# Optimization experiments

Hardware: AMD Instinct MI355X
Metric: run time of the kernel (lower is better)

The kernel has to match this reference:

```python
import jax, jax.numpy as jnp
import numpy as np

B, S, D = 4, 2048, 512
H, DK, DV = 8, 64, 64
DFF = 2048
LN_EPS = 1e-5


def _layernorm(x, g, b):
    mu = jnp.mean(x, axis=-1, keepdims=True)
    var = jnp.mean(jnp.square(x - mu), axis=-1, keepdims=True)
    return (x - mu) * jax.lax.rsqrt(var + LN_EPS) * g + b


def setup_inputs() -> dict:
    key = jax.random.key(0)
    ks = jax.random.split(key, 9)
    def xavier(k, shape):
        fan_out, fan_in = shape
        std = np.sqrt(2.0 / (fan_in + fan_out))
        return jax.random.normal(k, shape, jnp.float32) * std
    GELU_GAIN = 1.85
    return {
        "x": jax.random.normal(ks[0], (B, S, D), jnp.float32),
        "attention_mask": jax.random.randint(ks[1], (B, S), 0, 2).astype(bool),
        "Wq": xavier(ks[2], (H * DK, D)),
        "Wk": xavier(ks[3], (H * DK, D)),
        "Wv": xavier(ks[4], (H * DV, D)),
        "Wp": xavier(ks[5], (D, H * DV)),
        "W1": xavier(ks[6], (DFF, D)) * GELU_GAIN,
        "b1": jnp.zeros((DFF,), jnp.float32),
        "W2": xavier(ks[7], (D, DFF)),
        "b2": jnp.zeros((D,), jnp.float32),
        "ln1_g": jnp.ones((D,), jnp.float32),
        "ln1_b": jnp.zeros((D,), jnp.float32),
        "ln2_g": jnp.ones((D,), jnp.float32),
        "ln2_b": jnp.zeros((D,), jnp.float32),
    }


def reference(x, attention_mask, Wq, Wk, Wv, Wp, W1, b1, W2, b2,
              ln1_g, ln1_b, ln2_g, ln2_b):
    b, s, d = x.shape
    residual = x
    q = (x @ Wq.T).reshape(b, s, H, DK)  # [B,S,H,DK]
    k = (x @ Wk.T).reshape(b, s, H, DK)
    v = (x @ Wv.T).reshape(b, s, H, DV)
    score = jnp.einsum("bshd,bthd->bhst", q, k) * (DK ** -0.5)  # [B,H,S,S]
    # subtractive mask: score -= 100 * not(mask)
    score = score - 100.0 * (~attention_mask)[:, None, None, :].astype(score.dtype)
    p = jax.nn.softmax(score, axis=-1)
    ctx = jnp.einsum("bhst,bthd->bshd", p, v).reshape(b, s, H * DV)
    att = ctx @ Wp.T  # dropout p=0.1 is identity in eval
    h = _layernorm(att + residual, ln1_g, ln1_b)
    ff = jax.nn.gelu(h @ W1.T + b1, approximate=False) @ W2.T + b2
    out = _layernorm(ff + h, ln2_g, ln2_b)
    return out
```

## Files before the change

kernel.cpp:

```cpp
#include <hip/hip_runtime.h>
#include <cstdint>
#include <cstddef>

#define B_ 4
#define S_ 2048
#define D_ 512
#define H_ 8
#define DK_ 64
#define DFF_ 2048

using s16x8  = __attribute__((ext_vector_type(8))) short;
using bf16x8 = __attribute__((ext_vector_type(8))) __bf16;
using f32x4  = __attribute__((ext_vector_type(4))) float;

__device__ __forceinline__ short f2bf(float f) {
  unsigned u = __builtin_bit_cast(unsigned, f);
  u += 0x7FFFu + ((u >> 16) & 1u);
  return (short)(u >> 16);
}
__device__ __forceinline__ float bf2f(short s) {
  unsigned u = ((unsigned)(unsigned short)s) << 16;
  return __builtin_bit_cast(float, u);
}

__device__ __forceinline__ void gl2lds16(const void* g, void* l) {
  __builtin_amdgcn_global_load_lds(
      (const __attribute__((address_space(1))) void*)g,
      (__attribute__((address_space(3))) void*)l, 16, 0, 0);
}

__global__ __launch_bounds__(256)
void cvt_all(const float* __restrict__ x, const float* __restrict__ Wq,
             const float* __restrict__ Wk, const float* __restrict__ Wv,
             const float* __restrict__ Wp, const float* __restrict__ W1,
             const float* __restrict__ W2,
             short* __restrict__ xb, short* __restrict__ wqkv,
             short* __restrict__ wp, short* __restrict__ w1, short* __restrict__ w2) {
  int blk = blockIdx.x;
  const float* src; short* dst; int off;
  if (blk < 4096)      { src = x;  dst = xb;            off = blk; }
  else if (blk < 4352) { src = Wq; dst = wqkv;          off = blk - 4096; }
  else if (blk < 4608) { src = Wk; dst = wqkv + 262144; off = blk - 4352; }
  else if (blk < 4864) { src = Wv; dst = wqkv + 524288; off = blk - 4608; }
  else if (blk < 5120) { src = Wp; dst = wp;            off = blk - 4864; }
  else if (blk < 6144) { src = W1; dst = w1;            off = blk - 5120; }
  else                 { src = W2; dst = w2;            off = blk - 6144; }
  int i = (off * 256 + threadIdx.x) * 4;
  float4 v = *(const float4*)(src + i);
  *(short4*)(dst + i) = make_short4(f2bf(v.x), f2bf(v.y), f2bf(v.z), f2bf(v.w));
}

template <int MODE>
__global__ __launch_bounds__(256)
void gemm_bt(const short* __restrict__ A, const short* __restrict__ B,
             int M, int N, int K,
             const float* __restrict__ aux1,
             void* __restrict__ out0, void* __restrict__ out1, void* __restrict__ out2) {
  __shared__ alignas(16) short As[2][128][64];
  __shared__ alignas(16) short Bs[2][128][64];

  const int tid  = threadIdx.x;
  const int lane = tid & 63;
  const int wave = tid >> 6;
  const int quad = lane >> 4;
  const int l16  = lane & 15;
  const int wm   = (wave >> 1) * 64;
  const int wn   = (wave & 1) * 64;
  const int bm   = blockIdx.x * 128;
  const int bn   = blockIdx.y * 128;
  const int Kh   = K / gridDim.z;
  const int koff = blockIdx.z * Kh;

  const int srow8 = lane >> 3;
  const int pb    = lane & 7;

  f32x4 acc[4][4] = {};

  const int nt = Kh >> 6;

#pragma unroll
  for (int i = 0; i < 4; ++i) {
    const int rr = wave * 32 + i * 8 + srow8;
    const int cb = pb ^ (rr & 7);
    gl2lds16(A + (size_t)(bm + rr) * K + koff + cb * 8, &As[0][wave * 32 + i * 8][0]);
    gl2lds16(B + (size_t)(bn + rr) * K + koff + cb * 8, &Bs[0][wave * 32 + i * 8][0]);
  }
  __syncthreads();

  int cur = 0;
  for (int t = 0; t < nt; ++t) {
    if (t + 1 < nt) {
      const int kk = koff + (t + 1) * 64;
#pragma unroll
      for (int i = 0; i < 4; ++i) {
        const int rr = wave * 32 + i * 8 + srow8;
        const int cb = pb ^ (rr & 7);
        gl2lds16(A + (size_t)(bm + rr) * K + kk + cb * 8, &As[cur ^ 1][wave * 32 + i * 8][0]);
        gl2lds16(B + (size_t)(bn + rr) * K + kk + cb * 8, &Bs[cur ^ 1][wave * 32 + i * 8][0]);
      }
    }

#pragma unroll
    for (int c = 0; c < 2; ++c) {
      bf16x8 a[4], b[4];
#pragma unroll
      for (int i = 0; i < 4; ++i) {
        const int row = wm + i * 16 + l16;
        const int pba = (c * 4 + quad) ^ (row & 7);
        a[i] = __builtin_bit_cast(bf16x8, *(const s16x8*)&As[cur][row][pba * 8]);
      }
#pragma unroll
      for (int j = 0; j < 4; ++j) {
        const int row = wn + j * 16 + l16;
        const int pbb = (c * 4 + quad) ^ (row & 7);
        b[j] = __builtin_bit_cast(bf16x8, *(const s16x8*)&Bs[cur][row][pbb * 8]);
      }
#pragma unroll
      for (int i = 0; i < 4; ++i)
#pragma unroll
        for (int j = 0; j < 4; ++j)
          acc[i][j] = __builtin_amdgcn_mfma_f32_16x16x32_bf16(a[i], b[j], acc[i][j], 0, 0, 0);
    }

    __syncthreads();
    cur ^= 1;
  }

#pragma unroll
  for (int i = 0; i < 4; ++i) {
    const int m0 = bm + wm + i * 16 + quad * 4;
#pragma unroll
    for (int j = 0; j < 4; ++j) {
      const int n = bn + wn + j * 16 + l16;
      if constexpr (MODE == 0) {
        const int bb = m0 >> 11, ss0 = m0 & 2047;
        if (n < 512) {
          short4 pk = make_short4(f2bf(acc[i][j][0] * 0.18033688f), f2bf(acc[i][j][1] * 0.18033688f),
                                  f2bf(acc[i][j][2] * 0.18033688f), f2bf(acc[i][j][3] * 0.18033688f));
          *(short4*)((short*)out0 +
              ((((size_t)bb * H_ + (n >> 6)) * 64 + (n & 63)) * S_ + ss0)) = pk;
        } else if (n >= 1024) {
          const int nn = n - 1024;
          short4 pk = make_short4(f2bf(acc[i][j][0]), f2bf(acc[i][j][1]),
                                  f2bf(acc[i][j][2]), f2bf(acc[i][j][3]));
          *(short4*)((short*)out2 +
              ((((size_t)bb * H_ + (nn >> 6)) * 64 + (nn & 63)) * S_ + ss0)) = pk;
        } else {
          const int nn = n - 512;
          const size_t rowb = ((size_t)bb * H_ + (nn >> 6)) * S_ + ss0;
#pragma unroll
          for (int rr = 0; rr < 4; ++rr)
            ((short*)out1)[(rowb + rr) * 64 + (nn & 63)] = f2bf(acc[i][j][rr]);
        }
      } else if constexpr (MODE == 1) {
        float* dst = (float*)out0 + (size_t)blockIdx.z * M * N;
#pragma unroll
        for (int rr = 0; rr < 4; ++rr)
          dst[(size_t)(m0 + rr) * N + n] = acc[i][j][rr];
      } else {
#pragma unroll
        for (int rr = 0; rr < 4; ++rr) {
          float t = acc[i][j][rr] + aux1[n];
          float x2 = t * t;
          float t2 = t * (2.3022082f + 0.1029464f * x2);
          float e  = __builtin_amdgcn_exp2f(t2);
          float gl = t - t * __builtin_amdgcn_rcpf(1.0f + e);
          ((short*)out0)[(size_t)(m0 + rr) * N + n] = f2bf(gl);
        }
      }
    }
  }
}

__global__ __launch_bounds__(512)
void flash_attn_mfma(const short* __restrict__ QTg, const short* __restrict__ Kb,
                     const short* __restrict__ Vtg, const void* __restrict__ mraw,
                     short* __restrict__ ctxb) {
  __shared__ alignas(16) short Ks[64][64];
  __shared__ alignas(16) short Vt[64][64];
  __shared__ alignas(16) short Ps[8][32][64];
  __shared__ alignas(8) unsigned char mbits8[256];
  __shared__ unsigned red[8];

  int flat = (blockIdx.z * 8 + blockIdx.y) * 8 + blockIdx.x;
  flat = (flat & 7) * 32 + (flat >> 3);
  const int b = flat >> 6, h = (flat >> 3) & 7;
  const int q0 = (flat & 7) * 256;

  const int tid = threadIdx.x;
  const int w = tid >> 6, lane = tid & 63;
  const int quad = lane >> 4, l16 = lane & 15;
  const size_t base  = ((size_t)(b * H_ + h)) * S_ * DK_;
  const size_t baseT = ((size_t)(b * H_ + h)) * DK_ * S_;

  {
    const unsigned* mw = (const unsigned*)mraw;
    unsigned v = 0;
#pragma unroll
    for (int i = 0; i < 4; ++i) v |= mw[tid + i * 512];
#pragma unroll
    for (int s = 1; s < 64; s <<= 1) v |= __shfl_xor(v, s);
    if (lane == 0) red[w] = v;
    __syncthreads();
    unsigned f = red[0] | red[1] | red[2] | red[3] |
                 red[4] | red[5] | red[6] | red[7];
    if (tid < 256) {
      unsigned byte = 0;
#pragma unroll
      for (int j = 0; j < 8; ++j) {
        int t = tid * 8 + j;
        int gidx = b * S_ + t;
        int val;
        if ((f & ~1u) == 0u)            val = ((const int*)mraw)[gidx];
        else if (f == 0x3F800000u)      val = (((const float*)mraw)[gidx] != 0.0f);
        else                            val = ((const unsigned char*)mraw)[gidx];
        byte |= (val ? 1u : 0u) << j;
      }
      mbits8[tid] = (unsigned char)byte;
    }
  }

  bf16x8 qa[2][2];
#pragma unroll
  for (int st = 0; st < 2; ++st) {
    const int q = q0 + w * 32 + st * 16 + l16;
#pragma unroll
    for (int c = 0; c < 2; ++c) {
      s16x8 t;
#pragma unroll
      for (int j = 0; j < 8; ++j)
        t[j] = QTg[baseT + (size_t)(c * 32 + quad * 8 + j) * S_ + q];
      qa[st][c] = __builtin_bit_cast(bf16x8, t);
    }
  }

  f32x4 Oc[2][4] = {};
  float li[2] = {};
  const int swz = l16 & 7;

  const int r = tid >> 3, cc = tid & 7;
  const short* kp = Kb  + base  + (size_t)r * 64 + cc * 8;
  const short* vp = Vtg + baseT + (size_t)r * S_ + cc * 8;
  const int ch = ((cc ^ (r & 7)) << 3);

  s16x8 kr = *(const s16x8*)(kp);
  s16x8 vr = *(const s16x8*)(vp);

  for (int t0 = 0; t0 < S_; t0 += 64) {
    __syncthreads();
    *(s16x8*)&Ks[r][ch] = kr;
    *(s16x8*)&Vt[r][ch] = vr;
    __syncthreads();

    if (t0 + 64 < S_) {
      kr = *(const s16x8*)(kp + (size_t)(t0 + 64) * 64);
      vr = *(const s16x8*)(vp + (t0 + 64));
    }

    f32x4 sc[2][4] = {};
    __builtin_amdgcn_s_setprio(1);
#pragma unroll
    for (int c = 0; c < 2; ++c) {
#pragma unroll
      for (int jt = 0; jt < 4; ++jt) {
        bf16x8 kb = __builtin_bit_cast(bf16x8,
            *(const s16x8*)&Ks[jt * 16 + l16][((c * 4 + quad) ^ swz) << 3]);
        sc[0][jt] = __builtin_amdgcn_mfma_f32_16x16x32_bf16(kb, qa[0][c], sc[0][jt], 0, 0, 0);
        sc[1][jt] = __builtin_amdgcn_mfma_f32_16x16x32_bf16(kb, qa[1][c], sc[1][jt], 0, 0, 0);
      }
    }
    __builtin_amdgcn_s_setprio(0);

    const unsigned long long mball =
        *(const unsigned long long*)&mbits8[t0 >> 3];
#pragma unroll
    for (int jt = 0; jt < 4; ++jt) {
      const unsigned m16 = ((unsigned)(mball >> (jt * 16))) >> (quad * 4);
      const int pch = (((jt * 2 + (quad >> 1)) ^ swz) << 3) + (quad & 1) * 4;
#pragma unroll
      for (int st = 0; st < 2; ++st) {
        unsigned uu[4];
#pragma unroll
        for (int rr = 0; rr < 4; ++rr) {
          float pe = __builtin_amdgcn_exp2f(sc[st][jt][rr]);
          unsigned u = __builtin_bit_cast(unsigned, pe) & 0xFFFF0000u;
          u = ((m16 >> rr) & 1u) ? u : 0u;
          li[st] += __builtin_bit_cast(float, u);
          uu[rr] = u;
        }
        *(uint2*)&Ps[w][st * 16 + l16][pch] =
            make_uint2(__builtin_amdgcn_perm(uu[1], uu[0], 0x07060302u),
                       __builtin_amdgcn_perm(uu[3], uu[2], 0x07060302u));
      }
    }

    __builtin_amdgcn_s_setprio(1);
#pragma unroll
    for (int c = 0; c < 2; ++c) {
      bf16x8 pa0 = __builtin_bit_cast(bf16x8,
          *(const s16x8*)&Ps[w][l16][((c * 4 + quad) ^ swz) << 3]);
      bf16x8 pa1 = __builtin_bit_cast(bf16x8,
          *(const s16x8*)&Ps[w][16 + l16][((c * 4 + quad) ^ swz) << 3]);
#pragma unroll
      for (int dt = 0; dt < 4; ++dt) {
        bf16x8 vb = __builtin_bit_cast(bf16x8,
            *(const s16x8*)&Vt[dt * 16 + l16][((c * 4 + quad) ^ swz) << 3]);
        Oc[0][dt] = __builtin_amdgcn_mfma_f32_16x16x32_bf16(pa0, vb, Oc[0][dt], 0, 0, 0);
        Oc[1][dt] = __builtin_amdgcn_mfma_f32_16x16x32_bf16(pa1, vb, Oc[1][dt], 0, 0, 0);
      }
    }
    __builtin_amdgcn_s_setprio(0);
  }

#pragma unroll
  for (int st = 0; st < 2; ++st) {
    float l = li[st];
    l += __shfl_xor(l, 16);
    l += __shfl_xor(l, 32);
#pragma unroll
    for (int rr = 0; rr < 4; ++rr) {
      float lr = __shfl(l, quad * 4 + rr);
      float inv = 1.f / lr;
      const size_t row = (size_t)b * S_ + q0 + w * 32 + st * 16 + quad * 4 + rr;
#pragma unroll
      for (int dt = 0; dt < 4; ++dt)
        ctxb[row * (H_ * DK_) + h * 64 + dt * 16 + l16] = f2bf(Oc[st][dt][rr] * inv);
    }
  }
}

__global__ __launch_bounds__(256)
void ln_fused(const float* __restrict__ p0, const float* __restrict__ p1,
              const float* __restrict__ xres, const short* __restrict__ hres,
              const float* __restrict__ bias,
              const float* __restrict__ g, const float* __restrict__ bb,
              float* __restrict__ out32, short* __restrict__ outb) {
  const int wave = threadIdx.x >> 6, lane = threadIdx.x & 63;
  const int token = blockIdx.x * 4 + wave;
  const size_t off = (size_t)token * D_;
  const int c = lane * 8;

  float v[8];
  {
    float4 a0 = *(const float4*)(p0 + off + c);
    float4 a1 = *(const float4*)(p0 + off + c + 4);
    float4 b0 = *(const float4*)(p1 + off + c);
    float4 b1 = *(const float4*)(p1 + off + c + 4);
    v[0]=a0.x+b0.x; v[1]=a0.y+b0.y; v[2]=a0.z+b0.z; v[3]=a0.w+b0.w;
    v[4]=a1.x+b1.x; v[5]=a1.y+b1.y; v[6]=a1.z+b1.z; v[7]=a1.w+b1.w;
  }
  if (xres) {
    float4 x0 = *(const float4*)(xres + off + c);
    float4 x1 = *(const float4*)(xres + off + c + 4);
    v[0]+=x0.x; v[1]+=x0.y; v[2]+=x0.z; v[3]+=x0.w;
    v[4]+=x1.x; v[5]+=x1.y; v[6]+=x1.z; v[7]+=x1.w;
  }
  if (hres) {
    short4 h0 = *(const short4*)(hres + off + c);
    short4 h1 = *(const short4*)(hres + off + c + 4);
    v[0]+=bf2f(h0.x); v[1]+=bf2f(h0.y); v[2]+=bf2f(h0.z); v[3]+=bf2f(h0.w);
    v[4]+=bf2f(h1.x); v[5]+=bf2f(h1.y); v[6]+=bf2f(h1.z); v[7]+=bf2f(h1.w);
  }
  if (bias) {
    float4 c0 = *(const float4*)(bias + c);
    float4 c1 = *(const float4*)(bias + c + 4);
    v[0]+=c0.x; v[1]+=c0.y; v[2]+=c0.z; v[3]+=c0.w;
    v[4]+=c1.x; v[5]+=c1.y; v[6]+=c1.z; v[7]+=c1.w;
  }

  float sum = 0.f;
#pragma unroll
  for (int i = 0; i < 8; ++i) sum += v[i];
#pragma unroll
  for (int m = 1; m < 64; m <<= 1) sum += __shfl_xor(sum, m);
  float mu = sum * (1.0f / D_);
  float vs = 0.f;
#pragma unroll
  for (int i = 0; i < 8; ++i) { v[i] -= mu; vs += v[i] * v[i]; }
#pragma unroll
  for (int m = 1; m < 64; m <<= 1) vs += __shfl_xor(vs, m);
  float rstd = rsqrtf(vs * (1.0f / D_) + 1e-5f);
#pragma unroll
  for (int i = 0; i < 8; ++i) {
    float val = v[i] * rstd * g[c + i] + bb[c + i];
    if (out32) out32[off + c + i] = val;
    if (outb)  outb[off + c + i] = f2bf(val);
  }
}

constexpr size_t OFF_XB   = 0;
constexpr size_t OFF_WQKV = 8388608;
constexpr size_t OFF_WP   = 9961472;
constexpr size_t OFF_W1   = 10485760;
constexpr size_t OFF_W2   = 12582912;
constexpr size_t OFF_QT   = 14680064;
constexpr size_t OFF_K    = 23068672;
constexpr size_t OFF_VT   = 31457280;
constexpr size_t OFF_CTX  = 39845888;
constexpr size_t OFF_P0   = 48234496;
constexpr size_t OFF_P1   = 65011712;
constexpr size_t OFF_HB   = 81788928;
constexpr size_t OFF_FF1  = 14680064;
constexpr size_t WS_NEED  = 90177536;

extern "C" void kernel_launch(void* const* d_in, const int* in_sizes, int n_in,
                              void* d_out, int out_size, void* d_ws, size_t ws_size,
                              hipStream_t stream) {
  if (ws_size < WS_NEED) return;

  const float* x    = (const float*)d_in[0];
  const void*  msk  = d_in[1];
  const float* Wq   = (const float*)d_in[2];
  const float* Wk   = (const float*)d_in[3];
  const float* Wv   = (const float*)d_in[4];
  const float* Wp   = (const float*)d_in[5];
  const float* W1   = (const float*)d_in[6];
  const float* b1   = (const float*)d_in[7];
  const float* W2   = (const float*)d_in[8];
  const float* b2   = (const float*)d_in[9];
  const float* ln1g = (const float*)d_in[10];
  const float* ln1b = (const float*)d_in[11];
  const float* ln2g = (const float*)d_in[12];
  const float* ln2b = (const float*)d_in[13];

  char* ws = (char*)d_ws;
  short* xb    = (short*)(ws + OFF_XB);
  short* wqkv  = (short*)(ws + OFF_WQKV);
  short* Wpb   = (short*)(ws + OFF_WP);
  short* W1b   = (short*)(ws + OFF_W1);
  short* W2b   = (short*)(ws + OFF_W2);
  short* QTb   = (short*)(ws + OFF_QT);
  short* Kbh   = (short*)(ws + OFF_K);
  short* VTb   = (short*)(ws + OFF_VT);
  short* ctxb  = (short*)(ws + OFF_CTX);
  float* p0    = (float*)(ws + OFF_P0);
  short* hb    = (short*)(ws + OFF_HB);
  short* ff1b  = (short*)(ws + OFF_FF1);

  cvt_all<<<7168, 256, 0, stream>>>(x, Wq, Wk, Wv, Wp, W1, W2,
                                    xb, wqkv, Wpb, W1b, W2b);

  gemm_bt<0><<<dim3(64, 12, 1), 256, 0, stream>>>(xb, wqkv, 8192, 1536, 512,
                                                  nullptr, QTb, Kbh, VTb);

  flash_attn_mfma<<<dim3(S_ / 256, H_, B_), 512, 0, stream>>>(QTb, Kbh, VTb, msk, ctxb);

  gemm_bt<1><<<dim3(64, 4, 2), 256, 0, stream>>>(ctxb, Wpb, 8192, 512, 512,
                                                 nullptr, p0, nullptr, nullptr);

  ln_fused<<<2048, 256, 0, stream>>>(p0, p0 + (size_t)8192 * 512, x, nullptr, nullptr,
                                     ln1g, ln1b, nullptr, hb);

  gemm_bt<2><<<dim3(64, 16, 1), 256, 0, stream>>>(hb, W1b, 8192, 2048, 512,
                                                  b1, ff1b, nullptr, nullptr);

  gemm_bt<1><<<dim3(64, 4, 2), 256, 0, stream>>>(ff1b, W2b, 8192, 512, 2048,
                                                 nullptr, p0, nullptr, nullptr);

  ln_fused<<<2048, 256, 0, stream>>>(p0, p0 + (size_t)8192 * 512, nullptr, hb, b2,
                                     ln2g, ln2b, (float*)d_out, nullptr);
}
```

Measured before the change: 282.0 us.

## Add 256x256-tile GEMM kernel for QKV projection and FFN1

Adds a 512-thread GEMM kernel with 256x256 output tiles and 128x64 per-wave tiles, and uses it for the QKV projection and the first FFN GEMM. The epilogue is moved into a shared helper. Larger tiles raise arithmetic intensity and cut global and LDS traffic per FLOP. The cost is 64KB of LDS, more accumulator registers and fewer blocks (192 and 256) spread across the CUs, which can leave some CUs idle or lower occupancy.

```diff
diff --git a/kernel.cpp b/kernel.cpp
--- a/kernel.cpp
+++ b/kernel.cpp
@@ -51,6 +51,48 @@
 }
 
 template <int MODE>
+__device__ __forceinline__ void gemm_store(int m0, int n, const f32x4& a,
+                                           const float* __restrict__ aux1,
+                                           void* out0, void* out1, void* out2,
+                                           int M, int N, int bz) {
+  if constexpr (MODE == 0) {
+    const int bb = m0 >> 11, ss0 = m0 & 2047;
+    if (n < 512) {
+      short4 pk = make_short4(f2bf(a[0] * 0.18033688f), f2bf(a[1] * 0.18033688f),
+                              f2bf(a[2] * 0.18033688f), f2bf(a[3] * 0.18033688f));
+      *(short4*)((short*)out0 +
+          ((((size_t)bb * H_ + (n >> 6)) * 64 + (n & 63)) * S_ + ss0)) = pk;
+    } else if (n >= 1024) {
+      const int nn = n - 1024;
+      short4 pk = make_short4(f2bf(a[0]), f2bf(a[1]), f2bf(a[2]), f2bf(a[3]));
+      *(short4*)((short*)out2 +
+          ((((size_t)bb * H_ + (nn >> 6)) * 64 + (nn & 63)) * S_ + ss0)) = pk;
+    } else {
+      const int nn = n - 512;
+      const size_t rowb = ((size_t)bb * H_ + (nn >> 6)) * S_ + ss0;
+#pragma unroll
+      for (int rr = 0; rr < 4; ++rr)
+        ((short*)out1)[(rowb + rr) * 64 + (nn & 63)] = f2bf(a[rr]);
+    }
+  } else if constexpr (MODE == 1) {
+    float* dst = (float*)out0 + (size_t)bz * M * N;
+#pragma unroll
+    for (int rr = 0; rr < 4; ++rr)
+      dst[(size_t)(m0 + rr) * N + n] = a[rr];
+  } else {
+#pragma unroll
+    for (int rr = 0; rr < 4; ++rr) {
+      float t = a[rr] + aux1[n];
+      float x2 = t * t;
+      float t2 = t * (2.3022082f + 0.1029464f * x2);
+      float e  = __builtin_amdgcn_exp2f(t2);
+      float gl = t - t * __builtin_amdgcn_rcpf(1.0f + e);
+      ((short*)out0)[(size_t)(m0 + rr) * N + n] = f2bf(gl);
+    }
+  }
+}
+
+template <int MODE>
 __global__ __launch_bounds__(256)
 void gemm_bt(const short* __restrict__ A, const short* __restrict__ B,
              int M, int N, int K,
@@ -75,7 +117,6 @@
   const int pb    = lane & 7;
 
   f32x4 acc[4][4] = {};
-
   const int nt = Kh >> 6;
 
 #pragma unroll
@@ -106,14 +147,14 @@
 #pragma unroll
       for (int i = 0; i < 4; ++i) {
         const int row = wm + i * 16 + l16;
-        const int pba = (c * 4 + quad) ^ (row & 7);
-        a[i] = __builtin_bit_cast(bf16x8, *(const s16x8*)&As[cur][row][pba * 8]);
+        a[i] = __builtin_bit_cast(bf16x8,
+            *(const s16x8*)&As[cur][row][(((c * 4 + quad) ^ (row & 7))) * 8]);
       }
 #pragma unroll
       for (int j = 0; j < 4; ++j) {
         const int row = wn + j * 16 + l16;
-        const int pbb = (c * 4 + quad) ^ (row & 7);
-        b[j] = __builtin_bit_cast(bf16x8, *(const s16x8*)&Bs[cur][row][pbb * 8]);
+        b[j] = __builtin_bit_cast(bf16x8,
+            *(const s16x8*)&Bs[cur][row][(((c * 4 + quad) ^ (row & 7))) * 8]);
       }
 #pragma unroll
       for (int i = 0; i < 4; ++i)
@@ -130,45 +171,92 @@
   for (int i = 0; i < 4; ++i) {
     const int m0 = bm + wm + i * 16 + quad * 4;
 #pragma unroll
-    for (int j = 0; j < 4; ++j) {
-      const int n = bn + wn + j * 16 + l16;
-      if constexpr (MODE == 0) {
-        const int bb = m0 >> 11, ss0 = m0 & 2047;
-        if (n < 512) {
-          short4 pk = make_short4(f2bf(acc[i][j][0] * 0.18033688f), f2bf(acc[i][j][1] * 0.18033688f),
-                                  f2bf(acc[i][j][2] * 0.18033688f), f2bf(acc[i][j][3] * 0.18033688f));
-          *(short4*)((short*)out0 +
-              ((((size_t)bb * H_ + (n >> 6)) * 64 + (n & 63)) * S_ + ss0)) = pk;
-        } else if (n >= 1024) {
-          const int nn = n - 1024;
-          short4 pk = make_short4(f2bf(acc[i][j][0]), f2bf(acc[i][j][1]),
-                                  f2bf(acc[i][j][2]), f2bf(acc[i][j][3]));
-          *(short4*)((short*)out2 +
-              ((((size_t)bb * H_ + (nn >> 6)) * 64 + (nn & 63)) * S_ + ss0)) = pk;
-        } else {
-          const int nn = n - 512;
-          const size_t rowb = ((size_t)bb * H_ + (nn >> 6)) * S_ + ss0;
-#pragma unroll
-          for (int rr = 0; rr < 4; ++rr)
-            ((short*)out1)[(rowb + rr) * 64 + (nn & 63)] = f2bf(acc[i][j][rr]);
-        }
-      } else if constexpr (MODE == 1) {
-        float* dst = (float*)out0 + (size_t)blockIdx.z * M * N;
-#pragma unroll
-        for (int rr = 0; rr < 4; ++rr)
-          dst[(size_t)(m0 + rr) * N + n] = acc[i][j][rr];
-      } else {
-#pragma unroll
-        for (int rr = 0; rr < 4; ++rr) {
-          float t = acc[i][j][rr] + aux1[n];
-          float x2 = t * t;
-          float t2 = t * (2.3022082f + 0.1029464f * x2);
-          float e  = __builtin_amdgcn_exp2f(t2);
-          float gl = t - t * __builtin_amdgcn_rcpf(1.0f + e);
-          ((short*)out0)[(size_t)(m0 + rr) * N + n] = f2bf(gl);
-        }
-      }
-    }
+    for (int j = 0; j < 4; ++j)
+      gemm_store<MODE>(m0, bn + wn + j * 16 + l16, acc[i][j], aux1,
+                       out0, out1, out2, M, N, blockIdx.z);
+  }
+}
+
+template <int MODE>
+__global__ __launch_bounds__(512)
+void gemm256(const short* __restrict__ A, const short* __restrict__ B,
+             int M, int N, int K,
+             const float* __restrict__ aux1,
+             void* __restrict__ out0, void* __restrict__ out1, void* __restrict__ out2) {
+  __shared__ alignas(16) short As[2][256][64];
+  __shared__ alignas(16) short Bs[2][256][64];
+
+  const int tid  = threadIdx.x;
+  const int lane = tid & 63;
+  const int wave = tid >> 6;
+  const int quad = lane >> 4;
+  const int l16  = lane & 15;
+  const int wm   = (wave >> 2) * 128;
+  const int wn   = (wave & 3) * 64;
+  const int bm   = blockIdx.x * 256;
+  const int bn   = blockIdx.y * 256;
+
+  const int srow8 = lane >> 3;
+  const int pb    = lane & 7;
+
+  f32x4 acc[8][4] = {};
+  const int nt = K >> 6;
+
+#pragma unroll
+  for (int p = 0; p < 4; ++p) {
+    const int rr = p * 64 + wave * 8 + srow8;
+    const int cb = pb ^ (rr & 7);
+    gl2lds16(A + (size_t)(bm + rr) * K + cb * 8, &As[0][p * 64 + wave * 8][0]);
+    gl2lds16(B + (size_t)(bn + rr) * K + cb * 8, &Bs[0][p * 64 + wave * 8][0]);
+  }
+  __syncthreads();
+
+  int cur = 0;
+  for (int t = 0; t < nt; ++t) {
+    if (t + 1 < nt) {
+      const int kk = (t + 1) * 64;
+#pragma unroll
+      for (int p = 0; p < 4; ++p) {
+        const int rr = p * 64 + wave * 8 + srow8;
+        const int cb = pb ^ (rr & 7);
+        gl2lds16(A + (size_t)(bm + rr) * K + kk + cb * 8, &As[cur ^ 1][p * 64 + wave * 8][0]);
+        gl2lds16(B + (size_t)(bn + rr) * K + kk + cb * 8, &Bs[cur ^ 1][p * 64 + wave * 8][0]);
+      }
+    }
+
+#pragma unroll
+    for (int c = 0; c < 2; ++c) {
+      bf16x8 a[8], b[4];
+#pragma unroll
+      for (int i = 0; i < 8; ++i) {
+        const int row = wm + i * 16 + l16;
+        a[i] = __builtin_bit_cast(bf16x8,
+            *(const s16x8*)&As[cur][row][(((c * 4 + quad) ^ (row & 7))) * 8]);
+      }
+#pragma unroll
+      for (int j = 0; j < 4; ++j) {
+        const int row = wn + j * 16 + l16;
+        b[j] = __builtin_bit_cast(bf16x8,
+            *(const s16x8*)&Bs[cur][row][(((c * 4 + quad) ^ (row & 7))) * 8]);
+      }
+#pragma unroll
+      for (int i = 0; i < 8; ++i)
+#pragma unroll
+        for (int j = 0; j < 4; ++j)
+          acc[i][j] = __builtin_amdgcn_mfma_f32_16x16x32_bf16(a[i], b[j], acc[i][j], 0, 0, 0);
+    }
+
+    __syncthreads();
+    cur ^= 1;
+  }
+
+#pragma unroll
+  for (int i = 0; i < 8; ++i) {
+    const int m0 = bm + wm + i * 16 + quad * 4;
+#pragma unroll
+    for (int j = 0; j < 4; ++j)
+      gemm_store<MODE>(m0, bn + wn + j * 16 + l16, acc[i][j], aux1,
+                       out0, out1, out2, M, N, 0);
   }
 }
 
@@ -440,8 +528,8 @@
   cvt_all<<<7168, 256, 0, stream>>>(x, Wq, Wk, Wv, Wp, W1, W2,
                                     xb, wqkv, Wpb, W1b, W2b);
 
-  gemm_bt<0><<<dim3(64, 12, 1), 256, 0, stream>>>(xb, wqkv, 8192, 1536, 512,
-                                                  nullptr, QTb, Kbh, VTb);
+  gemm256<0><<<dim3(32, 6, 1), 512, 0, stream>>>(xb, wqkv, 8192, 1536, 512,
+                                                 nullptr, QTb, Kbh, VTb);
 
   flash_attn_mfma<<<dim3(S_ / 256, H_, B_), 512, 0, stream>>>(QTb, Kbh, VTb, msk, ctxb);
 
@@ -451,8 +539,8 @@
   ln_fused<<<2048, 256, 0, stream>>>(p0, p0 + (size_t)8192 * 512, x, nullptr, nullptr,
                                      ln1g, ln1b, nullptr, hb);
 
-  gemm_bt<2><<<dim3(64, 16, 1), 256, 0, stream>>>(hb, W1b, 8192, 2048, 512,
-                                                  b1, ff1b, nullptr, nullptr);
+  gemm256<2><<<dim3(32, 8, 1), 512, 0, stream>>>(hb, W1b, 8192, 2048, 512,
+                                                 b1, ff1b, nullptr, nullptr);
 
   gemm_bt<1><<<dim3(64, 4, 2), 256, 0, stream>>>(ff1b, W2b, 8192, 512, 2048,
                                                  nullptr, p0, nullptr, nullptr);
```

Measured after the change: 280.3 us (median of 3 runs). Within noise of the previous version (-0.6%).
